# Kernel optimization log

Hardware: AMD Instinct MI355X
Metric: run time of the kernel (lower is better)

The kernel has to match this reference:

```python
import jax, jax.numpy as jnp
import numpy as np

HIDDEN = 1024
HEADS = 16
HEAD_DIM = HIDDEN // HEADS
ROTARY_PCT = 0.25
ROTARY_DIM = int(HEAD_DIM * ROTARY_PCT)  # 16
BASE = 10000.0
SCALE = HEAD_DIM ** -0.5
EPS = 1e-8


def _rotate_half(x):
    h = x.shape[-1] // 2
    return jnp.concatenate([-x[..., h:], x[..., :h]], axis=-1)


def _apply_rope(q, k, position_ids):
    # q, k: [B, H, S, D]; NeoX-style partial rotary on first ROTARY_DIM dims
    inv_freq = 1.0 / (BASE ** (jnp.arange(0, ROTARY_DIM, 2, dtype=jnp.float32) / ROTARY_DIM))
    freqs = position_ids.astype(jnp.float32)[:, None] * inv_freq[None, :]  # [S, rd/2]
    emb = jnp.concatenate([freqs, freqs], axis=-1)  # [S, rd]
    cos = jnp.cos(emb)[None, None, :, :]
    sin = jnp.sin(emb)[None, None, :, :]

    def rot(x):
        x_rot, x_pass = x[..., :ROTARY_DIM], x[..., ROTARY_DIM:]
        x_rot = x_rot * cos + _rotate_half(x_rot) * sin
        return jnp.concatenate([x_rot, x_pass], axis=-1)

    return rot(q), rot(k)


def _ka_scan(attn_weights, value):
    # attn_weights: [B, H, S, S] causal softmax; value: [B, H, S, D]
    # A[0] = V[0]; A[i] = renorm(attn_weights[i, :i]) @ A[:i]
    S = value.shape[2]
    idx = jnp.arange(S)

    def step(a_buf, i):
        w = attn_weights[:, :, i, :]                      # [B, H, S]
        w = jnp.where(idx[None, None, :] < i, w, 0.0)     # strict past only
        w = w / (jnp.sum(w, axis=-1, keepdims=True) + EPS)
        a_i = jnp.einsum('bhs,bhsd->bhd', w, a_buf)
        a_i = jnp.where(i == 0, value[:, :, 0, :], a_i)
        a_buf = jax.lax.dynamic_update_slice(a_buf, a_i[:, :, None, :], (0, 0, i, 0))
        return a_buf, None

    a_buf, _ = jax.lax.scan(step, jnp.zeros_like(value), jnp.arange(S))
    return a_buf


def setup_inputs() -> dict:
    key = jax.random.key(0)
    k1, k2, k3 = jax.random.split(key, 3)
    B, S = 2, 2048
    hidden_states = jax.random.normal(k1, (B, S, HIDDEN), dtype=jnp.float32)
    position_ids = jnp.arange(S, dtype=jnp.int32)
    Wqkv = jax.random.normal(k2, (HIDDEN, 3 * HIDDEN), dtype=jnp.float32) / np.sqrt(HIDDEN)
    bqkv = jnp.zeros((3 * HIDDEN,), dtype=jnp.float32)
    Wd = jax.random.normal(k3, (HIDDEN, HIDDEN), dtype=jnp.float32) / np.sqrt(HIDDEN)
    bd = jnp.zeros((HIDDEN,), dtype=jnp.float32)
    return {"hidden_states": hidden_states, "position_ids": position_ids,
            "Wqkv": Wqkv, "bqkv": bqkv, "Wd": Wd, "bd": bd}


def reference(hidden_states, position_ids, Wqkv, bqkv, Wd, bd):
    B, S, _ = hidden_states.shape
    qkv = hidden_states @ Wqkv + bqkv                       # [B, S, 3*hidden]
    qkv = qkv.reshape(B, S, 3, HEADS, HEAD_DIM).transpose(2, 0, 3, 1, 4)
    query, key, value = qkv[0], qkv[1], qkv[2]              # [B, H, S, D]
    query, key = _apply_rope(query, key, position_ids)

    scores = jnp.einsum('bhqd,bhkd->bhqk', query, key) * SCALE
    causal = jnp.tril(jnp.ones((S, S), dtype=bool))
    scores = jnp.where(causal[None, None], scores, -jnp.inf)
    attn_weights = jax.nn.softmax(scores, axis=-1)          # [B, H, S, S]

    attn_output = _ka_scan(attn_weights, value)             # [B, H, S, D]
    attn_output = attn_output.transpose(0, 2, 1, 3).reshape(B, S, HIDDEN)
    return attn_output @ Wd + bd
```

## Files before the change

### kernel.cpp

```cpp
#include <hip/hip_runtime.h>

#define S_ 2048
#define EPSF 1e-8f
#define SCALEF 0.125f

typedef short bf16x8 __attribute__((ext_vector_type(8)));
typedef float f32x4 __attribute__((ext_vector_type(4)));

__device__ __forceinline__ unsigned short f2bf(float f){
  unsigned int u = __float_as_uint(f);
  u = (u + 0x7fffu + ((u >> 16) & 1u)) >> 16;
  return (unsigned short)u;
}
__device__ __forceinline__ float bf2f(unsigned short h){
  return __uint_as_float(((unsigned int)h) << 16);
}
__device__ __forceinline__ unsigned short f2bf_trunc(float f){
  return (unsigned short)(__float_as_uint(f) >> 16);
}

__global__ void k_prep(const float* __restrict__ hs, const float* __restrict__ Wqkv,
                       const float* __restrict__ bqkv,
                       unsigned short* __restrict__ Ab,
                       unsigned short* __restrict__ WT,
                       float* __restrict__ v0){
  __shared__ float t[32][33];
  __shared__ float red[4][64];
  int bid = blockIdx.x;
  if (bid < 4096){
    int i = (bid * 256 + threadIdx.x) * 4;
    float4 v = *(const float4*)(hs + i);
    ushort4 o; o.x=f2bf(v.x); o.y=f2bf(v.y); o.z=f2bf(v.z); o.w=f2bf(v.w);
    *(ushort4*)(Ab + i) = o;
  } else if (bid < 6144){
    int q = bid - 4096;
    int nt = q & 63, kt = q >> 6;
    int tx = threadIdx.x & 31, ty = threadIdx.x >> 5;
    #pragma unroll
    for (int r = 0; r < 32; r += 8)
      t[ty + r][tx] = Wqkv[(size_t)(kt*32 + ty + r)*3072 + nt*32 + tx];
    __syncthreads();
    #pragma unroll
    for (int r = 0; r < 32; r += 8)
      WT[(size_t)(nt*32 + ty + r)*1024 + kt*32 + tx] = f2bf(t[tx][ty + r]);
  } else {
    int bh = bid - 6144; int b = bh >> 4;
    int d = threadIdx.x & 63, kc = threadIdx.x >> 6;
    const float* x = hs + (size_t)b * S_ * 1024;
    int col = 2048 + (bh & 15)*64 + d;
    float acc = 0.f;
    #pragma unroll 8
    for (int k = kc*256; k < kc*256 + 256; ++k)
      acc = fmaf(x[k], Wqkv[(size_t)k*3072 + col], acc);
    red[kc][d] = acc;
    __syncthreads();
    if (kc == 0)
      v0[bh*64 + d] = red[0][d] + red[1][d] + red[2][d] + red[3][d] + bqkv[col];
  }
}

#define GSTRIDE 72
__launch_bounds__(256)
__global__ void k_gemm_qk(const unsigned short* __restrict__ Ab,
                          const unsigned short* __restrict__ WT,
                          const float* __restrict__ bqkv,
                          const int* __restrict__ pos_ids,
                          unsigned short* __restrict__ Qb,
                          unsigned short* __restrict__ Kb){
  __shared__ unsigned short At[128*GSTRIDE];
  __shared__ unsigned short Bt[128*GSTRIDE];
  const int m0 = blockIdx.y * 128, n0 = blockIdx.x * 128;
  const int w = threadIdx.x >> 6, l = threadIdx.x & 63;
  const int wr = w >> 1, wc = w & 1;
  f32x4 acc[4][4];
  #pragma unroll
  for (int i = 0; i < 4; ++i)
    #pragma unroll
    for (int j = 0; j < 4; ++j) acc[i][j] = (f32x4){0.f,0.f,0.f,0.f};

  const int srow = threadIdx.x >> 1;
  const int sseg = (threadIdx.x & 1) * 2;

  for (int kt = 0; kt < 1024; kt += 32){
    int4 va0 = *(const int4*)(Ab + (size_t)(m0+srow)*1024 + kt + sseg*8);
    int4 va1 = *(const int4*)(Ab + (size_t)(m0+srow)*1024 + kt + sseg*8 + 8);
    int4 vb0 = *(const int4*)(WT + (size_t)(n0+srow)*1024 + kt + sseg*8);
    int4 vb1 = *(const int4*)(WT + (size_t)(n0+srow)*1024 + kt + sseg*8 + 8);
    *(int4*)&At[srow*GSTRIDE + sseg*8]     = va0;
    *(int4*)&At[srow*GSTRIDE + sseg*8 + 8] = va1;
    *(int4*)&Bt[srow*GSTRIDE + sseg*8]     = vb0;
    *(int4*)&Bt[srow*GSTRIDE + sseg*8 + 8] = vb1;
    __syncthreads();
    bf16x8 af[4], bf[4];
    #pragma unroll
    for (int i = 0; i < 4; ++i)
      af[i] = *(const bf16x8*)&At[(wr*64 + i*16 + (l&15))*GSTRIDE + (l>>4)*8];
    #pragma unroll
    for (int j = 0; j < 4; ++j)
      bf[j] = *(const bf16x8*)&Bt[(wc*64 + j*16 + (l&15))*GSTRIDE + (l>>4)*8];
    #pragma unroll
    for (int i = 0; i < 4; ++i)
      #pragma unroll
      for (int j = 0; j < 4; ++j)
        acc[i][j] = __builtin_amdgcn_mfma_f32_16x16x32_bf16(af[i], bf[j], acc[i][j], 0, 0, 0);
    __syncthreads();
  }
  #pragma unroll
  for (int i = 0; i < 4; ++i){
    #pragma unroll
    for (int j = 0; j < 4; ++j){
      #pragma unroll
      for (int r = 0; r < 4; ++r){
        int m = m0 + wr*64 + i*16 + (l>>4)*4 + r;
        int n = n0 + wc*64 + j*16 + (l&15);
        float v = acc[i][j][r] + bqkv[n];
        if (j == 0){
          float partner = __shfl_xor(v, 8);
          int s = m & 2047;
          float pos = (float)pos_ids[s];
          float fr = exp2f(-1.6609640474436813f * (float)(l & 7));
          float th = pos * fr;
          float sn = __sinf(th), cn = __cosf(th);
          v = ((l & 8) == 0) ? (v*cn - partner*sn) : (v*cn + partner*sn);
        }
        int b = m >> 11, s2 = m & 2047;
        int tsel = n >> 10; int nq = n & 1023;
        int h = nq >> 6, d = nq & 63;
        unsigned short* dst = tsel ? Kb : Qb;
        dst[((size_t)(b*16 + h)*S_ + s2)*64 + d] = f2bf(v);
      }
    }
  }
}

#define KST2 66
#define EST 68
__launch_bounds__(256, 4)
__global__ void k_scores(const unsigned short* __restrict__ Qb,
                         const unsigned short* __restrict__ Kb,
                         unsigned short* __restrict__ Eg,
                         float* __restrict__ rinvg){
  __shared__ unsigned short Ks[2][64*KST2];
  __shared__ unsigned short Es[4][16*EST];
  __shared__ float dsh[4][16];
  const int bi = blockIdx.x >> 5, bh = blockIdx.x & 31;
  const unsigned short* Qh = Qb + (size_t)bh * S_ * 64;
  const unsigned short* Kh = Kb + (size_t)bh * S_ * 64;
  const int tid = threadIdx.x, w = tid >> 6, l = tid & 63;
  const int lq = l & 15, lh = l >> 4;
  const unsigned short* qp = Qh + (size_t)(bi*64 + w*16 + lq)*64 + lh*8;
  bf16x8 qf0 = *(const bf16x8*)(qp);
  bf16x8 qf1 = *(const bf16x8*)(qp + 32);
  float dacc[4] = {0.f,0.f,0.f,0.f};
  unsigned short* Etile0 = Eg + ((size_t)bh*528 + (size_t)(bi*(bi+1)/2))*4096;
  const int srow = tid >> 2, sc = (tid & 3)*16;

  {
    const unsigned short* src = Kh + (size_t)srow*64 + sc;
    *(int4*)&Ks[0][srow*KST2 + sc]     = *(const int4*)(src);
    *(int4*)&Ks[0][srow*KST2 + sc + 8] = *(const int4*)(src + 8);
  }
  __syncthreads();

  for (int bj = 0; bj <= bi; ++bj){
    const int cur = bj & 1;
    int4 nk0, nk1;
    if (bj < bi){
      const unsigned short* src = Kh + (size_t)((bj+1)*64 + srow)*64 + sc;
      nk0 = *(const int4*)(src);
      nk1 = *(const int4*)(src + 8);
    }
    unsigned short* Et = Etile0 + (size_t)bj*4096 + w*1024;
    const bool diag = (bj == bi);
    #pragma unroll
    for (int ct = 0; ct < 4; ++ct){
      bf16x8 b0 = *(const bf16x8*)&Ks[cur][(ct*16 + lq)*KST2 + lh*8];
      bf16x8 b1 = *(const bf16x8*)&Ks[cur][(ct*16 + lq)*KST2 + 32 + lh*8];
      f32x4 a = (f32x4){0.f,0.f,0.f,0.f};
      a = __builtin_amdgcn_mfma_f32_16x16x32_bf16(qf0, b0, a, 0, 0, 0);
      a = __builtin_amdgcn_mfma_f32_16x16x32_bf16(qf1, b1, a, 0, 0, 0);
      #pragma unroll
      for (int r = 0; r < 4; ++r){
        float e = __expf(a[r] * SCALEF);
        unsigned short eb = f2bf_trunc(e);
        int rrow = lh*4 + r, col = ct*16 + lq;
        Es[w][rrow*EST + col] = eb;
        float ev = bf2f(eb);
        int grow = w*16 + rrow;
        if (!diag || col < grow) dacc[r] += ev;
        if (diag && col == grow) dsh[w][rrow] = ev;
      }
    }
    #pragma unroll
    for (int it = 0; it < 2; ++it){
      int row = it*8 + (l >> 3), eo = (l & 7)*8;
      *(int4*)(Et + row*64 + eo) = *(const int4*)&Es[w][row*EST + eo];
    }
    if (bj < bi){
      *(int4*)&Ks[cur^1][srow*KST2 + sc]     = nk0;
      *(int4*)&Ks[cur^1][srow*KST2 + sc + 8] = nk1;
    }
    __syncthreads();
  }
  #pragma unroll
  for (int r = 0; r < 4; ++r){
    float d = dacc[r];
    #pragma unroll
    for (int mm = 1; mm < 16; mm <<= 1) d += __shfl_xor(d, mm);
    float dE = dsh[w][lh*4 + r];
    float den = fmaf(EPSF, d + dE, d);
    float rv = 1.0f / den;
    if (lq == 0)
      rinvg[(size_t)bh*S_ + bi*64 + w*16 + lh*4 + r] = rv;
  }
}

__global__ __launch_bounds__(512)
__attribute__((amdgpu_waves_per_eu(2, 2)))
void k_recur3(const unsigned short* __restrict__ Eg,
              const float* __restrict__ rinvg,
              float* __restrict__ c_c,
              float* __restrict__ c_g){
  __shared__ float Pa[512];
  __shared__ float rso[512];
  __shared__ float csl[2][64];
  const int bh = blockIdx.x & 31, s = blockIdx.x >> 5;
  const unsigned short* Eh = Eg + (size_t)bh * 528 * 4096;
  const int tid = threadIdx.x, w = tid >> 6, l = tid & 63;
  const int lq = l & 15, lh = l >> 4;

  Pa[tid] = 0.f;
  rso[tid] = rinvg[(size_t)bh*S_ + (s + 4*w)*64 + l];
  __syncthreads();

  bf16x8 er[8];
  if (w == 0){
    const unsigned short* dt = Eh + ((size_t)(s*(s+1)/2) + s)*4096 + l*64;
    #pragma unroll
    for (int eb = 0; eb < 8; ++eb) er[eb] = *(const bf16x8*)(dt + eb*8);
  }

  bf16x8 dA0[5], dA1[5], dB0[5], dB1[5];
  bf16x8 ug0, ug1;
  const int lastc = s + 28;

  auto load_def = [&](int BJ, bf16x8 (&D0)[5], bf16x8 (&D1)[5]){
    int o0 = (BJ >= s) ? (((BJ - s) >> 2) + 1) : 0;
    int ex = (((BJ + 1) & 3) == s) ? 1 : 0;
    int nd = (8 - o0 - ex) * 4;
    if (w >= 1){
      #pragma unroll
      for (int k = 0; k < 5; ++k){
        int t = (w - 1) + k*7;
        if (t < nd){
          int ob = o0 + ex + (t >> 2);
          int bi = s + 4*ob;
          const unsigned short* tp =
              Eh + ((size_t)(bi*(bi+1)/2) + BJ)*4096 + (size_t)(t & 3)*1024;
          D0[k] = *(const bf16x8*)(tp + lq*64 + lh*8);
          D1[k] = *(const bf16x8*)(tp + lq*64 + 32 + lh*8);
        }
      }
      if (ex && w <= 4){
        int bi = BJ + 1;
        const unsigned short* tp =
            Eh + ((size_t)(bi*(bi+1)/2) + BJ)*4096 + (size_t)(w-1)*1024;
        ug0 = *(const bf16x8*)(tp + lq*64 + lh*8);
        ug1 = *(const bf16x8*)(tp + lq*64 + 32 + lh*8);
      }
    }
  };

  auto fold_def = [&](int BJP, bf16x8 (&D0)[5], bf16x8 (&D1)[5], int buf){
    int o0 = (BJP >= s) ? (((BJP - s) >> 2) + 1) : 0;
    int ex = (((BJP + 1) & 3) == s) ? 1 : 0;
    int nd = (8 - o0 - ex) * 4;
    if (w >= 1 && nd > 0){
      bf16x8 dc0 = (bf16x8){0,0,0,0,0,0,0,0};
      bf16x8 dc1 = (bf16x8){0,0,0,0,0,0,0,0};
      if (lq == 0){
        #pragma unroll
        for (int e = 0; e < 8; ++e){
          dc0[e] = (short)f2bf(csl[buf][lh*8 + e]);
          dc1[e] = (short)f2bf(csl[buf][32 + lh*8 + e]);
        }
      }
      #pragma unroll
      for (int k = 0; k < 5; ++k){
        int t = (w - 1) + k*7;
        if (t < nd){
          f32x4 o = (f32x4){0.f,0.f,0.f,0.f};
          o = __builtin_amdgcn_mfma_f32_16x16x32_bf16(D0[k], dc0, o, 0, 0, 0);
          o = __builtin_amdgcn_mfma_f32_16x16x32_bf16(D1[k], dc1, o, 0, 0, 0);
          if (lq == 0){
            int ob = o0 + ex + (t >> 2);
            float* base = Pa + ob*64 + (t & 3)*16 + lh*4;
            float4 v = *(float4*)base;
            v.x += o[0]; v.y += o[1]; v.z += o[2]; v.w += o[3];
            *(float4*)base = v;
          }
        }
      }
    }
  };

  auto iter = [&](int BJ, bf16x8 (&DL0)[5], bf16x8 (&DL1)[5],
                          bf16x8 (&DF0)[5], bf16x8 (&DF1)[5]){
    const int cur = BJ & 1;
    load_def(BJ, DL0, DL1);
    const int ex = (((BJ + 1) & 3) == s) ? 1 : 0;
    if (w == 0){
      if ((BJ & 3) == s){
        const int rr = l;
        const int o = (BJ - s) >> 2;
        float rinv = rso[o*64 + rr];
        float Pl = Pa[o*64 + rr];
        float cval = 0.f;
        #pragma unroll
        for (int eb = 0; eb < 8; ++eb){
          #pragma unroll
          for (int e = 0; e < 8; ++e){
            int r = eb*8 + e;
            float t2 = Pl * rinv;
            float cr = __uint_as_float(
                (unsigned)__builtin_amdgcn_readlane(__float_as_uint(t2), r));
            if (BJ == 0 && r == 0) cr = 1.0f;
            if (rr == r) cval = cr;
            float m = (rr > r) ? bf2f((unsigned short)er[eb][e]) : 0.f;
            Pl = fmaf(m, cr, Pl);
          }
        }
        csl[cur][rr] = cval;
        __hip_atomic_store((unsigned*)(c_c + (size_t)bh*S_ + BJ*64 + rr),
                           __float_as_uint(cval),
                           __ATOMIC_RELAXED, __HIP_MEMORY_SCOPE_AGENT);
        c_g[((size_t)(bh >> 4)*S_ + (BJ*64 + rr))*16 + (bh & 15)] = cval;
        int bn = BJ + 4;
        if (bn <= lastc){
          const unsigned short* dt =
              Eh + ((size_t)(bn*(bn+1)/2) + bn)*4096 + l*64;
          #pragma unroll
          for (int eb = 0; eb < 8; ++eb) er[eb] = *(const bf16x8*)(dt + eb*8);
        }
      } else {
        const unsigned* pp = (const unsigned*)(c_c + (size_t)bh*S_ + BJ*64 + l);
        unsigned v = __hip_atomic_load(pp, __ATOMIC_RELAXED,
                                       __HIP_MEMORY_SCOPE_AGENT);
        while (!__all(v != 0u)){
          __builtin_amdgcn_s_sleep(2);
          v = __hip_atomic_load(pp, __ATOMIC_RELAXED,
                                __HIP_MEMORY_SCOPE_AGENT);
        }
        csl[cur][l] = __uint_as_float(v);
      }
    } else if (BJ >= 1){
      fold_def(BJ - 1, DF0, DF1, cur ^ 1);
    }
    __syncthreads();
    if (ex && w >= 1 && w <= 4){
      bf16x8 uc0 = (bf16x8){0,0,0,0,0,0,0,0};
      bf16x8 uc1 = (bf16x8){0,0,0,0,0,0,0,0};
      if (lq == 0){
        #pragma unroll
        for (int e = 0; e < 8; ++e){
          uc0[e] = (short)f2bf(csl[cur][lh*8 + e]);
          uc1[e] = (short)f2bf(csl[cur][32 + lh*8 + e]);
        }
      }
      f32x4 o = (f32x4){0.f,0.f,0.f,0.f};
      o = __builtin_amdgcn_mfma_f32_16x16x32_bf16(ug0, uc0, o, 0, 0, 0);
      o = __builtin_amdgcn_mfma_f32_16x16x32_bf16(ug1, uc1, o, 0, 0, 0);
      if (lq == 0){
        int ou = (BJ + 1 - s) >> 2;
        float* base = Pa + ou*64 + (w-1)*16 + lh*4;
        float4 v = *(float4*)base;
        v.x += o[0]; v.y += o[1]; v.z += o[2]; v.w += o[3];
        *(float4*)base = v;
      }
    }
    __syncthreads();
  };

  for (int bj = 0; bj <= lastc; bj += 2){
    iter(bj,     dA0, dA1, dB0, dB1);
    if (bj + 1 <= lastc)
      iter(bj+1, dB0, dB1, dA0, dA1);
  }
}

__global__ void k_u(const float* __restrict__ v0, const float* __restrict__ Wd,
                    float* __restrict__ U){
  int bh = blockIdx.x; int h = bh & 15;
  __shared__ float vsh[64];
  if (threadIdx.x < 64) vsh[threadIdx.x] = v0[bh*64 + threadIdx.x];
  __syncthreads();
  for (int n = threadIdx.x; n < 1024; n += 256){
    float acc = 0.f;
    #pragma unroll 8
    for (int d = 0; d < 64; ++d) acc = fmaf(vsh[d], Wd[(size_t)(h*64 + d)*1024 + n], acc);
    U[(size_t)bh*1024 + n] = acc;
  }
}

__global__ void k_out(const float* __restrict__ c_g, const float* __restrict__ U,
                      const float* __restrict__ bd, float* __restrict__ out){
  int bs = blockIdx.x; int b = bs >> 11;
  __shared__ float ch[16];
  if (threadIdx.x < 16) ch[threadIdx.x] = c_g[(size_t)bs*16 + threadIdx.x];
  __syncthreads();
  int n = threadIdx.x * 4;
  float4 acc = *(const float4*)(bd + n);
  #pragma unroll
  for (int h = 0; h < 16; ++h){
    float cc = ch[h];
    float4 u = *(const float4*)(U + ((size_t)(b*16 + h))*1024 + n);
    acc.x = fmaf(cc, u.x, acc.x); acc.y = fmaf(cc, u.y, acc.y);
    acc.z = fmaf(cc, u.z, acc.z); acc.w = fmaf(cc, u.w, acc.w);
  }
  *(float4*)(out + (size_t)bs*1024 + n) = acc;
}

extern "C" void kernel_launch(void* const* d_in, const int* in_sizes, int n_in,
                              void* d_out, int out_size, void* d_ws, size_t ws_size,
                              hipStream_t stream) {
  const float* hs   = (const float*)d_in[0];
  const int*   pos  = (const int*)d_in[1];
  const float* Wqkv = (const float*)d_in[2];
  const float* bqkv = (const float*)d_in[3];
  const float* Wd   = (const float*)d_in[4];
  const float* bd   = (const float*)d_in[5];
  float* out = (float*)d_out;

  char* ws = (char*)d_ws;
  unsigned short* Ab = (unsigned short*)(ws);
  unsigned short* WT = (unsigned short*)(ws + (8u<<20));
  unsigned short* Qb = (unsigned short*)(ws + (12u<<20));
  unsigned short* Kb = (unsigned short*)(ws + (20u<<20));
  float* v0   = (float*)(ws + (28u<<20));
  float* c_g  = (float*)(ws + (28u<<20) + 0x10000);
  float* U    = (float*)(ws + (28u<<20) + 0x50000);
  float* rinvg= (float*)(ws + (28u<<20) + 0x80000);
  float* c_c  = (float*)(ws + (28u<<20) + 0xC0000);
  unsigned short* Eg = (unsigned short*)(ws + (29u<<20));

  k_prep   <<<6176, 256, 0, stream>>>(hs, Wqkv, bqkv, Ab, WT, v0);
  k_gemm_qk<<<dim3(16, 32), 256, 0, stream>>>(Ab, WT, bqkv, pos, Qb, Kb);
  k_scores <<<1024, 256, 0, stream>>>(Qb, Kb, Eg, rinvg);
  hipMemsetAsync(c_c, 0, 32 * S_ * sizeof(float), stream);
  k_recur3 <<<128, 512, 0, stream>>>(Eg, rinvg, c_c, c_g);
  k_u      <<<32, 256, 0, stream>>>(v0, Wd, U);
  k_out    <<<4096, 256, 0, stream>>>(c_g, U, bd, out);
}
```

Before: 208.4 us.

## Fuse U projection into prep kernel and load GEMM tiles via global_load_lds

The separate k_u kernel, which projects the first value row through Wd, is folded into the last blocks of k_prep, removing one launch and the v0 round trip through global memory. The QK projection GEMM now stages A and B tiles with direct global-to-LDS loads (global_load_lds, 16 bytes) into an unpadded 32-wide tile instead of loading into registers and storing to LDS. This removes register staging, but the unpadded LDS layout may cause bank conflicts on the fragment reads.

```diff
diff --git a/kernel.cpp b/kernel.cpp
--- a/kernel.cpp
+++ b/kernel.cpp
@@ -19,13 +19,18 @@
   return (unsigned short)(__float_as_uint(f) >> 16);
 }
 
+#define GLD16(g, l) __builtin_amdgcn_global_load_lds( \
+    (const __attribute__((address_space(1))) unsigned int*)(g), \
+    (__attribute__((address_space(3))) unsigned int*)(l), 16, 0, 0)
+
 __global__ void k_prep(const float* __restrict__ hs, const float* __restrict__ Wqkv,
-                       const float* __restrict__ bqkv,
+                       const float* __restrict__ bqkv, const float* __restrict__ Wd,
                        unsigned short* __restrict__ Ab,
                        unsigned short* __restrict__ WT,
-                       float* __restrict__ v0){
+                       float* __restrict__ U){
   __shared__ float t[32][33];
   __shared__ float red[4][64];
+  __shared__ float vsh[64];
   int bid = blockIdx.x;
   if (bid < 4096){
     int i = (bid * 256 + threadIdx.x) * 4;
@@ -44,10 +49,10 @@
     for (int r = 0; r < 32; r += 8)
       WT[(size_t)(nt*32 + ty + r)*1024 + kt*32 + tx] = f2bf(t[tx][ty + r]);
   } else {
-    int bh = bid - 6144; int b = bh >> 4;
+    int bh = bid - 6144; int b = bh >> 4, h = bh & 15;
     int d = threadIdx.x & 63, kc = threadIdx.x >> 6;
     const float* x = hs + (size_t)b * S_ * 1024;
-    int col = 2048 + (bh & 15)*64 + d;
+    int col = 2048 + h*64 + d;
     float acc = 0.f;
     #pragma unroll 8
     for (int k = kc*256; k < kc*256 + 256; ++k)
@@ -55,11 +60,19 @@
     red[kc][d] = acc;
     __syncthreads();
     if (kc == 0)
-      v0[bh*64 + d] = red[0][d] + red[1][d] + red[2][d] + red[3][d] + bqkv[col];
-  }
-}
-
-#define GSTRIDE 72
+      vsh[d] = red[0][d] + red[1][d] + red[2][d] + red[3][d] + bqkv[col];
+    __syncthreads();
+    for (int n = threadIdx.x; n < 1024; n += 256){
+      float a2 = 0.f;
+      #pragma unroll 8
+      for (int dd = 0; dd < 64; ++dd)
+        a2 = fmaf(vsh[dd], Wd[(size_t)(h*64 + dd)*1024 + n], a2);
+      U[(size_t)bh*1024 + n] = a2;
+    }
+  }
+}
+
+#define BK 32
 __launch_bounds__(256)
 __global__ void k_gemm_qk(const unsigned short* __restrict__ Ab,
                           const unsigned short* __restrict__ WT,
@@ -67,37 +80,34 @@
                           const int* __restrict__ pos_ids,
                           unsigned short* __restrict__ Qb,
                           unsigned short* __restrict__ Kb){
-  __shared__ unsigned short At[128*GSTRIDE];
-  __shared__ unsigned short Bt[128*GSTRIDE];
+  __shared__ unsigned short At[128*BK];
+  __shared__ unsigned short Bt[128*BK];
   const int m0 = blockIdx.y * 128, n0 = blockIdx.x * 128;
   const int w = threadIdx.x >> 6, l = threadIdx.x & 63;
   const int wr = w >> 1, wc = w & 1;
+  const int lq = l & 15, lh = l >> 4;
   f32x4 acc[4][4];
   #pragma unroll
   for (int i = 0; i < 4; ++i)
     #pragma unroll
     for (int j = 0; j < 4; ++j) acc[i][j] = (f32x4){0.f,0.f,0.f,0.f};
 
-  const int srow = threadIdx.x >> 1;
-  const int sseg = (threadIdx.x & 1) * 2;
-
-  for (int kt = 0; kt < 1024; kt += 32){
-    int4 va0 = *(const int4*)(Ab + (size_t)(m0+srow)*1024 + kt + sseg*8);
-    int4 va1 = *(const int4*)(Ab + (size_t)(m0+srow)*1024 + kt + sseg*8 + 8);
-    int4 vb0 = *(const int4*)(WT + (size_t)(n0+srow)*1024 + kt + sseg*8);
-    int4 vb1 = *(const int4*)(WT + (size_t)(n0+srow)*1024 + kt + sseg*8 + 8);
-    *(int4*)&At[srow*GSTRIDE + sseg*8]     = va0;
-    *(int4*)&At[srow*GSTRIDE + sseg*8 + 8] = va1;
-    *(int4*)&Bt[srow*GSTRIDE + sseg*8]     = vb0;
-    *(int4*)&Bt[srow*GSTRIDE + sseg*8 + 8] = vb1;
+  const int srow = l >> 2;
+  const int scol = (l & 3) * 8;
+
+  for (int kt = 0; kt < 1024; kt += BK){
+    GLD16(Ab + (size_t)(m0 + w*32 +      srow)*1024 + kt + scol, &At[(w*32)*BK]);
+    GLD16(Ab + (size_t)(m0 + w*32 + 16 + srow)*1024 + kt + scol, &At[(w*32+16)*BK]);
+    GLD16(WT + (size_t)(n0 + w*32 +      srow)*1024 + kt + scol, &Bt[(w*32)*BK]);
+    GLD16(WT + (size_t)(n0 + w*32 + 16 + srow)*1024 + kt + scol, &Bt[(w*32+16)*BK]);
     __syncthreads();
     bf16x8 af[4], bf[4];
     #pragma unroll
     for (int i = 0; i < 4; ++i)
-      af[i] = *(const bf16x8*)&At[(wr*64 + i*16 + (l&15))*GSTRIDE + (l>>4)*8];
+      af[i] = *(const bf16x8*)&At[(wr*64 + i*16 + lq)*BK + lh*8];
     #pragma unroll
     for (int j = 0; j < 4; ++j)
-      bf[j] = *(const bf16x8*)&Bt[(wc*64 + j*16 + (l&15))*GSTRIDE + (l>>4)*8];
+      bf[j] = *(const bf16x8*)&Bt[(wc*64 + j*16 + lq)*BK + lh*8];
     #pragma unroll
     for (int i = 0; i < 4; ++i)
       #pragma unroll
@@ -388,20 +398,6 @@
   }
 }
 
-__global__ void k_u(const float* __restrict__ v0, const float* __restrict__ Wd,
-                    float* __restrict__ U){
-  int bh = blockIdx.x; int h = bh & 15;
-  __shared__ float vsh[64];
-  if (threadIdx.x < 64) vsh[threadIdx.x] = v0[bh*64 + threadIdx.x];
-  __syncthreads();
-  for (int n = threadIdx.x; n < 1024; n += 256){
-    float acc = 0.f;
-    #pragma unroll 8
-    for (int d = 0; d < 64; ++d) acc = fmaf(vsh[d], Wd[(size_t)(h*64 + d)*1024 + n], acc);
-    U[(size_t)bh*1024 + n] = acc;
-  }
-}
-
 __global__ void k_out(const float* __restrict__ c_g, const float* __restrict__ U,
                       const float* __restrict__ bd, float* __restrict__ out){
   int bs = blockIdx.x; int b = bs >> 11;
@@ -436,18 +432,16 @@
   unsigned short* WT = (unsigned short*)(ws + (8u<<20));
   unsigned short* Qb = (unsigned short*)(ws + (12u<<20));
   unsigned short* Kb = (unsigned short*)(ws + (20u<<20));
-  float* v0   = (float*)(ws + (28u<<20));
   float* c_g  = (float*)(ws + (28u<<20) + 0x10000);
   float* U    = (float*)(ws + (28u<<20) + 0x50000);
   float* rinvg= (float*)(ws + (28u<<20) + 0x80000);
   float* c_c  = (float*)(ws + (28u<<20) + 0xC0000);
   unsigned short* Eg = (unsigned short*)(ws + (29u<<20));
 
-  k_prep   <<<6176, 256, 0, stream>>>(hs, Wqkv, bqkv, Ab, WT, v0);
+  k_prep   <<<6176, 256, 0, stream>>>(hs, Wqkv, bqkv, Wd, Ab, WT, U);
   k_gemm_qk<<<dim3(16, 32), 256, 0, stream>>>(Ab, WT, bqkv, pos, Qb, Kb);
   k_scores <<<1024, 256, 0, stream>>>(Qb, Kb, Eg, rinvg);
   hipMemsetAsync(c_c, 0, 32 * S_ * sizeof(float), stream);
   k_recur3 <<<128, 512, 0, stream>>>(Eg, rinvg, c_c, c_g);
-  k_u      <<<32, 256, 0, stream>>>(v0, Wd, U);
   k_out    <<<4096, 256, 0, stream>>>(c_g, U, bd, out);
 }
```

After: 201.8 us. 3.1% less time.
